# Kernel tuning notes

Hardware: AMD Instinct MI355X
Metric: run time of the kernel (lower is better)

## Reference

```python
import jax, jax.numpy as jnp
import numpy as np

N_NODES = 512
STATE_DIM = 32
MESSAGE_DIM = 32
H_MSG = 64
H_RO = 64
N_STEPS = 5


def setup_inputs() -> dict:
    key = jax.random.key(0)
    ks = jax.random.split(key, 20)
    s = 0.01  # torch init: normal(0, 0.01) weights, zero biases
    d, m = STATE_DIM, MESSAGE_DIM
    inp = {
        "J": jax.random.normal(ks[0], (N_NODES, N_NODES), jnp.float32),
        "b": jax.random.normal(ks[1], (N_NODES,), jnp.float32),
        # message-passing MLP
        "mp_W1": jax.random.normal(ks[2], (H_MSG, 2 * d + 3), jnp.float32) * s,
        "mp_b1": jnp.zeros((H_MSG,), jnp.float32),
        "mp_W2": jax.random.normal(ks[3], (H_MSG, H_MSG), jnp.float32) * s,
        "mp_b2": jnp.zeros((H_MSG,), jnp.float32),
        "mp_W3": jax.random.normal(ks[4], (m, H_MSG), jnp.float32) * s,
        "mp_b3": jnp.zeros((m,), jnp.float32),
        # GRU (input = state_dim + message_dim, hidden = state_dim); gate order r,z,n
        "gru_Wih": jax.random.normal(ks[5], (3 * d, d + m), jnp.float32) * 0.1,
        "gru_Whh": jax.random.normal(ks[6], (3 * d, d), jnp.float32) * 0.1,
        "gru_bih": jax.random.normal(ks[7], (3 * d,), jnp.float32) * 0.1,
        "gru_bhh": jax.random.normal(ks[8], (3 * d,), jnp.float32) * 0.1,
        # readout MLP
        "r_W1": jax.random.normal(ks[9], (H_RO, d), jnp.float32) * s,
        "r_b1": jnp.zeros((H_RO,), jnp.float32),
        "r_W2": jax.random.normal(ks[10], (H_RO, H_RO), jnp.float32) * s,
        "r_b2": jnp.zeros((H_RO,), jnp.float32),
        "r_W3": jax.random.normal(ks[11], (2, H_RO), jnp.float32) * s,
        "r_b3": jnp.zeros((2,), jnp.float32),
    }
    return inp


def reference(J, b, mp_W1, mp_b1, mp_W2, mp_b2, mp_W3, mp_b3,
              gru_Wih, gru_Whh, gru_bih, gru_bhh,
              r_W1, r_b1, r_W2, r_b2, r_W3, r_b3):
    n = J.shape[0]
    d = gru_Whh.shape[1]
    # split first message-layer weight by input segments to avoid building [n,n,2d+3]
    Wi, Wj = mp_W1[:, :d], mp_W1[:, d:2 * d]          # [H, d]
    wJ, wbi, wbj = mp_W1[:, 2 * d], mp_W1[:, 2 * d + 1], mp_W1[:, 2 * d + 2]  # [H]

    def step(h, _):
        # pre[i, j, :] = W1 @ cat(h_i, h_j, J_ij, b_i, b_j) + b1
        pre = ((h @ Wi.T)[:, None, :] + (h @ Wj.T)[None, :, :]
               + J[:, :, None] * wJ + b[:, None, None] * wbi
               + b[None, :, None] * wbj + mp_b1)          # [n, n, H]
        m1 = jax.nn.relu(pre)
        m2 = jax.nn.relu(m1 @ mp_W2.T + mp_b2)            # [n, n, H]
        msg = jax.nn.relu(m2 @ mp_W3.T + mp_b3)           # [n, n, M]
        msg_sum = msg.sum(axis=0)                         # sum over senders i -> [n, M]
        # GRU cell over all nodes (torch GRU, gate order r,z,n)
        x = jnp.concatenate([h, msg_sum], axis=-1)        # [n, d+M]
        gi = x @ gru_Wih.T + gru_bih                      # [n, 3d]
        gh = h @ gru_Whh.T + gru_bhh                      # [n, 3d]
        i_r, i_z, i_n = jnp.split(gi, 3, axis=-1)
        h_r, h_z, h_n = jnp.split(gh, 3, axis=-1)
        r = jax.nn.sigmoid(i_r + h_r)
        z = jax.nn.sigmoid(i_z + h_z)
        n_g = jnp.tanh(i_n + r * h_n)
        h_new = (1.0 - z) * n_g + z * h
        return h_new, None

    h0 = jnp.zeros((n, d), J.dtype)
    h, _ = jax.lax.scan(step, h0, None, length=N_STEPS)
    y = jax.nn.relu(h @ r_W1.T + r_b1)
    y = jax.nn.relu(y @ r_W2.T + r_b2)
    y = jax.nn.relu(y @ r_W3.T + r_b3)                    # [n, 2]
    return jax.nn.sigmoid(y)
```

## Files before the change

### kernel.cpp

```cpp
#include <hip/hip_runtime.h>
#include <math.h>

#define NN 512
#define SD 32
#define HM 64

typedef _Float16 f16x8 __attribute__((ext_vector_type(8)));
typedef float floatx4 __attribute__((ext_vector_type(4)));
typedef unsigned uintx4 __attribute__((ext_vector_type(4)));

#define OFF_HBS   0
#define OFF_M2L   73728
#define OFF_MSUM  92160
#define OFF_HPREV 93184
#define OFF_HS    93440
#define OFF_MSG   93696
#define OFF_GI    93952
#define OFF_GH    94720
#define LDS_TOTAL 95488

__device__ __forceinline__ float sigmoidf_(float x) {
    return 1.0f / (1.0f + __expf(-x));
}
__device__ __forceinline__ unsigned pkrtz(float a, float b) {
    unsigned r;
    asm("v_cvt_pkrtz_f16_f32 %0, %1, %2" : "=v"(r) : "v"(a), "v"(b));
    return r;
}
__device__ __forceinline__ unsigned pk_add(unsigned a, unsigned b) {
    unsigned r;
    asm("v_pk_add_f16 %0, %1, %2" : "=v"(r) : "v"(a), "v"(b));
    return r;
}
__device__ __forceinline__ unsigned pk_fma(unsigned a, unsigned b, unsigned c) {
    unsigned r;
    asm("v_pk_fma_f16 %0, %1, %2, %3" : "=v"(r) : "v"(a), "v"(b), "v"(c));
    return r;
}
__device__ __forceinline__ unsigned pk_relu(unsigned a) {
    unsigned r, z = 0u;
    asm("v_pk_max_f16 %0, %1, %2" : "=v"(r) : "v"(a), "v"(z));
    return r;
}

struct PParams {
    const float *J, *b, *mpW1, *mpb1, *mpW2, *mpW3, *Wih, *Whh, *rW1, *rW2;
    float *JT, *W1T, *WihT, *WhhT, *rW1T, *rW2T;
    unsigned *w2p, *w3p, *wjp, *hb0, *hjp0;
};

__global__ __launch_bounds__(256) void prep_kernel(PParams pp)
{
    __shared__ float tile[32][33];
    const int tid = threadIdx.x;
    const int b   = blockIdx.x;
    {
        int bx = b & 15, by = b >> 4;
        int tx = tid & 31, ty = tid >> 5;
        #pragma unroll
        for (int r = 0; r < 32; r += 8)
            tile[ty + r][tx] = pp.J[(by * 32 + ty + r) * NN + bx * 32 + tx];
        __syncthreads();
        #pragma unroll
        for (int r = 0; r < 32; r += 8)
            pp.JT[(bx * 32 + ty + r) * NN + by * 32 + tx] = tile[tx][ty + r];
    }
    if (b == 0 && tid < 64) {
        int l = tid, qq = l >> 4, cc = l & 15;
        for (int f = 0; f < 2; ++f)
            for (int t4 = 0; t4 < 4; ++t4) {
                const float* src = pp.mpW2 + (t4 * 16 + cc) * 64 + f * 32 + qq * 8;
                unsigned* dst = pp.w2p + ((f * 4 + t4) * 64 + l) * 4;
                for (int i = 0; i < 4; ++i) dst[i] = pkrtz(src[2 * i], src[2 * i + 1]);
            }
        for (int f = 0; f < 2; ++f)
            for (int t2 = 0; t2 < 2; ++t2) {
                const float* src = pp.mpW3 + (t2 * 16 + cc) * 64 + f * 32 + qq * 8;
                unsigned* dst = pp.w3p + ((f * 2 + t2) * 64 + l) * 4;
                for (int i = 0; i < 4; ++i) dst[i] = pkrtz(src[2 * i], src[2 * i + 1]);
            }
        for (int s = 0; s < 2; ++s) {
            unsigned* dst = pp.wjp + (s * 64 + l) * 4;
            for (int i = 0; i < 4; ++i) {
                int r0 = qq * 8 + 2 * i + s * 32;
                dst[i] = pkrtz(pp.mpW1[r0 * 67 + 64], pp.mpW1[(r0 + 1) * 67 + 64]);
            }
        }
    }
    if (b == 1)
        for (int n = tid; n < 64 * 67; n += 256) {
            int cc = n / 67, d = n % 67;
            pp.W1T[d * 64 + cc] = pp.mpW1[n];
        }
    if (b == 2)
        for (int n = tid; n < 96 * 64; n += 256)
            pp.WihT[(n & 63) * 96 + (n >> 6)] = pp.Wih[n];
    if (b == 3)
        for (int n = tid; n < 96 * 32; n += 256)
            pp.WhhT[(n & 31) * 96 + (n >> 5)] = pp.Whh[n];
    if (b == 4) {
        for (int n = tid; n < 64 * 32; n += 256)
            pp.rW1T[(n & 31) * 64 + (n >> 5)] = pp.rW1[n];
        for (int n = tid; n < 64 * 64; n += 256)
            pp.rW2T[(n & 63) * 64 + (n >> 6)] = pp.rW2[n];
    }
    if (b >= 16 && b < 144) {
        int jj = (b - 16) * 4 + (tid >> 6);
        int cc = tid & 63;
        float bj = pp.b[jj];
        float sj = bj * pp.mpW1[cc * 67 + 66] + pp.mpb1[cc];
        float si = bj * pp.mpW1[cc * 67 + 65];
        float sjp = __shfl(sj, cc ^ 1);
        float sip = __shfl(si, cc ^ 1);
        if (!(cc & 1)) {
            pp.hjp0[jj * 32 + (cc >> 1)] = pkrtz(sj, sjp);
            pp.hb0[jj * 32 + (cc >> 1)]  = pkrtz(si, sip);
        }
    }
}

struct SParams {
    const unsigned *hbR;  unsigned *hbW;
    const unsigned *hjR;  unsigned *hjW;
    const float *hR;      float *hW;
    const float *JT, *W1T, *WihT, *WhhT, *bih, *bhh, *mpb2, *mpb3, *b, *mpb1;
    const float *rW1T, *rW2T, *rW3, *rb1, *rb2, *rb3;
    const unsigned *w2p, *w3p, *wjp;
    float *out;
    int hzero, rdout;
};

__global__ __launch_bounds__(512, 1) void step_kernel(SParams s)
{
    extern __shared__ __align__(16) char smem[];
    char* hbS = smem + OFF_HBS;
    float (*msum)[32]   = (float(*)[32])(smem + OFF_MSUM);
    float (*hPrevS)[32] = (float(*)[32])(smem + OFF_HPREV);
    float (*hS)[32]     = (float(*)[32])(smem + OFF_HS);
    float (*msgS)[32]   = (float(*)[32])(smem + OFF_MSG);
    float (*giS)[96]    = (float(*)[96])(smem + OFF_GI);
    float (*ghS)[96]    = (float(*)[96])(smem + OFF_GH);

    const int tid  = threadIdx.x;
    const int lane = tid & 63;
    const int wave = tid >> 6;
    const int nsel = wave >> 2;
    const int nw   = wave & 3;
    const int j    = blockIdx.x * 2 + nsel;
    const int q    = lane >> 4;
    const int c    = lane & 15;
    char* m2Lw = smem + OFF_M2L + wave * 2304;

    {
        uintx4 cr[8];
        const uintx4* gp = (const uintx4*)s.hbR;
        #pragma unroll
        for (int k = 0; k < 8; ++k) cr[k] = gp[k * 512 + tid];
        #pragma unroll
        for (int k = 0; k < 8; ++k) {
            int row = k * 64 + (tid >> 3);
            *(uintx4*)(hbS + row * 144 + (tid & 7) * 16) = cr[k];
        }
    }
    if (tid < 64 && !s.hzero)
        hPrevS[tid >> 5][tid & 31] = s.hR[blockIdx.x * 64 + tid];
    __syncthreads();

    f16x8 Aw2[2][4], Aw3[2][2];
    #pragma unroll
    for (int f = 0; f < 2; ++f)
        #pragma unroll
        for (int t4 = 0; t4 < 4; ++t4)
            Aw2[f][t4] = __builtin_bit_cast(f16x8,
                ((const uintx4*)s.w2p)[(f * 4 + t4) * 64 + lane]);
    #pragma unroll
    for (int f = 0; f < 2; ++f)
        #pragma unroll
        for (int t2 = 0; t2 < 2; ++t2)
            Aw3[f][t2] = __builtin_bit_cast(f16x8,
                ((const uintx4*)s.w3p)[(f * 2 + t2) * 64 + lane]);
    uintx4 wja = ((const uintx4*)s.wjp)[lane];
    uintx4 wjb = ((const uintx4*)s.wjp)[64 + lane];
    uintx4 hja = ((const uintx4*)s.hjR)[j * 8 + q];
    uintx4 hjb = ((const uintx4*)s.hjR)[j * 8 + 4 + q];

    floatx4 b2i[4], b3i[2];
    #pragma unroll
    for (int t4 = 0; t4 < 4; ++t4)
        #pragma unroll
        for (int r = 0; r < 4; ++r) b2i[t4][r] = s.mpb2[t4 * 16 + q * 4 + r];
    #pragma unroll
    for (int t2 = 0; t2 < 2; ++t2)
        #pragma unroll
        for (int r = 0; r < 4; ++r) b3i[t2][r] = s.mpb3[t2 * 16 + q * 4 + r];

    const float jA = s.JT[j * NN + (8 * q + nw) * 16 + c];
    const float jB = s.JT[j * NN + (8 * q + 4 + nw) * 16 + c];

    float accf[2][4];
    #pragma unroll
    for (int t2 = 0; t2 < 2; ++t2)
        #pragma unroll
        for (int r = 0; r < 4; ++r) accf[t2][r] = 0.0f;

    auto edge_group = [&](int G, float Jv) {
        const char* rb = hbS + (G * 16 + c) * 144;
        uintx4 vlo = *(const uintx4*)(rb + q * 16);
        uintx4 vhi = *(const uintx4*)(rb + 64 + q * 16);
        const unsigned Jp = pkrtz(Jv, Jv);

        uintx4 a0u, a1u;
        #pragma unroll
        for (int i = 0; i < 4; ++i) {
            a0u[i] = pk_relu(pk_fma(Jp, wja[i], pk_add(vlo[i], hja[i])));
            a1u[i] = pk_relu(pk_fma(Jp, wjb[i], pk_add(vhi[i], hjb[i])));
        }
        f16x8 B0 = __builtin_bit_cast(f16x8, a0u);
        f16x8 B1 = __builtin_bit_cast(f16x8, a1u);

        floatx4 c1[4];
        #pragma unroll
        for (int t4 = 0; t4 < 4; ++t4) {
            c1[t4] = __builtin_amdgcn_mfma_f32_16x16x32_f16(Aw2[0][t4], B0, b2i[t4], 0, 0, 0);
            c1[t4] = __builtin_amdgcn_mfma_f32_16x16x32_f16(Aw2[1][t4], B1, c1[t4], 0, 0, 0);
        }
        #pragma unroll
        for (int t4 = 0; t4 < 4; ++t4) {
            unsigned p0 = pkrtz(fmaxf(c1[t4][0], 0.f), fmaxf(c1[t4][1], 0.f));
            unsigned p1 = pkrtz(fmaxf(c1[t4][2], 0.f), fmaxf(c1[t4][3], 0.f));
            *(uint2*)(m2Lw + c * 144 + t4 * 32 + q * 8) = make_uint2(p0, p1);
        }
        uintx4 rlo = *(const uintx4*)(m2Lw + c * 144 + q * 16);
        uintx4 rhi = *(const uintx4*)(m2Lw + c * 144 + 64 + q * 16);
        f16x8 B2lo = __builtin_bit_cast(f16x8, rlo);
        f16x8 B2hi = __builtin_bit_cast(f16x8, rhi);

        floatx4 c2[2];
        #pragma unroll
        for (int t2 = 0; t2 < 2; ++t2) {
            c2[t2] = __builtin_amdgcn_mfma_f32_16x16x32_f16(Aw3[0][t2], B2lo, b3i[t2], 0, 0, 0);
            c2[t2] = __builtin_amdgcn_mfma_f32_16x16x32_f16(Aw3[1][t2], B2hi, c2[t2], 0, 0, 0);
        }
        #pragma unroll
        for (int t2 = 0; t2 < 2; ++t2)
            #pragma unroll
            for (int r = 0; r < 4; ++r)
                accf[t2][r] += fmaxf(c2[t2][r], 0.0f);
    };

    #pragma unroll
    for (int k = 0; k < 4; ++k) {
        edge_group(8 * k + nw,     __shfl(jA, k * 16 + c));
        edge_group(8 * k + 4 + nw, __shfl(jB, k * 16 + c));
    }

    #pragma unroll
    for (int m = 1; m < 16; m <<= 1)
        #pragma unroll
        for (int t2 = 0; t2 < 2; ++t2)
            #pragma unroll
            for (int r = 0; r < 4; ++r)
                accf[t2][r] += __shfl_xor(accf[t2][r], m);
    if (c == 0) {
        #pragma unroll
        for (int t2 = 0; t2 < 2; ++t2)
            #pragma unroll
            for (int r = 0; r < 4; ++r)
                msum[wave][t2 * 16 + q * 4 + r] = accf[t2][r];
    }
    __syncthreads();

    if (tid < 64) {
        int node = tid >> 5, d = tid & 31;
        msgS[node][d] = msum[node * 4 + 0][d] + msum[node * 4 + 1][d] +
                        msum[node * 4 + 2][d] + msum[node * 4 + 3][d];
    }
    __syncthreads();

    if (tid < 192) {
        int node = tid / 96, r = tid % 96;
        float a  = s.bih[r];
        float bb = s.bhh[r];
        if (!s.hzero) {
            #pragma unroll
            for (int k = 0; k < 32; ++k) {
                float hv = hPrevS[node][k];
                a  = fmaf(hv, s.WihT[k * 96 + r], a);
                bb = fmaf(hv, s.WhhT[k * 96 + r], bb);
            }
        }
        #pragma unroll
        for (int k = 0; k < 32; ++k)
            a = fmaf(msgS[node][k], s.WihT[(32 + k) * 96 + r], a);
        giS[node][r] = a; ghS[node][r] = bb;
    }
    __syncthreads();

    if (tid < 64) {
        int node = tid >> 5, d = tid & 31;
        float r  = sigmoidf_(giS[node][d] + ghS[node][d]);
        float z  = sigmoidf_(giS[node][32 + d] + ghS[node][32 + d]);
        float ng = tanhf(giS[node][64 + d] + r * ghS[node][64 + d]);
        float hold = s.hzero ? 0.0f : hPrevS[node][d];
        float hv = (1.0f - z) * ng + z * hold;
        hS[node][d] = hv;
        s.hW[blockIdx.x * 64 + tid] = hv;
    }
    __syncthreads();

    if (!s.rdout) {
        if (tid < 128) {
            int node = tid >> 6, cc = tid & 63;
            int jj = blockIdx.x * 2 + node;
            float bj = s.b[jj];
            float si = bj * s.W1T[65 * 64 + cc];
            float sj = bj * s.W1T[66 * 64 + cc] + s.mpb1[cc];
            #pragma unroll
            for (int d = 0; d < 32; ++d) {
                float hv = hS[node][d];
                si = fmaf(hv, s.W1T[d * 64 + cc], si);
                sj = fmaf(hv, s.W1T[(32 + d) * 64 + cc], sj);
            }
            float sip = __shfl(si, lane ^ 1);
            float sjp = __shfl(sj, lane ^ 1);
            if (!(cc & 1)) {
                s.hbW[jj * 32 + (cc >> 1)] = pkrtz(si, sip);
                s.hjW[jj * 32 + (cc >> 1)] = pkrtz(sj, sjp);
            }
        }
    } else {
        if (wave < 2) {
            int node = wave;
            int jj = blockIdx.x * 2 + node;
            float y1 = s.rb1[lane];
            #pragma unroll
            for (int k = 0; k < 32; ++k)
                y1 = fmaf(hS[node][k], s.rW1T[k * 64 + lane], y1);
            y1 = fmaxf(y1, 0.0f);
            float y2 = s.rb2[lane];
            #pragma unroll
            for (int k = 0; k < 64; ++k)
                y2 = fmaf(__shfl(y1, k), s.rW2T[k * 64 + lane], y2);
            y2 = fmaxf(y2, 0.0f);
            float y3 = (lane < 2) ? s.rb3[lane] : 0.0f;
            #pragma unroll
            for (int k = 0; k < 64; ++k) {
                float v = __shfl(y2, k);
                if (lane < 2) y3 = fmaf(v, s.rW3[lane * 64 + k], y3);
            }
            if (lane < 2) s.out[jj * 2 + lane] = sigmoidf_(y3);
        }
    }
}

extern "C" void kernel_launch(void* const* d_in, const int* in_sizes, int n_in,
                              void* d_out, int out_size, void* d_ws, size_t ws_size,
                              hipStream_t stream)
{
    float* ws = (float*)d_ws;

    const float* J    = (const float*)d_in[0];
    const float* b    = (const float*)d_in[1];
    const float* mpW1 = (const float*)d_in[2];
    const float* mpb1 = (const float*)d_in[3];
    const float* mpW2 = (const float*)d_in[4];
    const float* mpb2 = (const float*)d_in[5];
    const float* mpW3 = (const float*)d_in[6];
    const float* mpb3 = (const float*)d_in[7];
    const float* Wih  = (const float*)d_in[8];
    const float* Whh  = (const float*)d_in[9];
    const float* bih  = (const float*)d_in[10];
    const float* bhh  = (const float*)d_in[11];
    const float* rW1  = (const float*)d_in[12];
    const float* rb1  = (const float*)d_in[13];
    const float* rW2  = (const float*)d_in[14];
    const float* rb2  = (const float*)d_in[15];
    const float* rW3  = (const float*)d_in[16];
    const float* rb3  = (const float*)d_in[17];

    float*    JT   = ws;
    float*    W1T  = ws + 262144;
    float*    WihT = ws + 266432;
    float*    WhhT = ws + 272576;
    float*    rW1T = ws + 275648;
    float*    rW2T = ws + 277696;
    unsigned* w2p  = (unsigned*)(ws + 281792);
    unsigned* w3p  = (unsigned*)(ws + 283840);
    unsigned* wjp  = (unsigned*)(ws + 284864);
    unsigned* hb0  = (unsigned*)(ws + 285376);
    unsigned* hb1  = (unsigned*)(ws + 301760);
    unsigned* hj0  = (unsigned*)(ws + 318144);
    unsigned* hj1  = (unsigned*)(ws + 334528);
    float*    h0   = ws + 350912;
    float*    h1   = ws + 367296;

    PParams pp;
    pp.J = J; pp.b = b; pp.mpW1 = mpW1; pp.mpb1 = mpb1; pp.mpW2 = mpW2;
    pp.mpW3 = mpW3; pp.Wih = Wih; pp.Whh = Whh; pp.rW1 = rW1; pp.rW2 = rW2;
    pp.JT = JT; pp.W1T = W1T; pp.WihT = WihT; pp.WhhT = WhhT;
    pp.rW1T = rW1T; pp.rW2T = rW2T;
    pp.w2p = w2p; pp.w3p = w3p; pp.wjp = wjp; pp.hb0 = hb0; pp.hjp0 = hj0;

    (void)hipFuncSetAttribute((const void*)step_kernel,
                              hipFuncAttributeMaxDynamicSharedMemorySize, LDS_TOTAL);

    prep_kernel<<<dim3(256), dim3(256), 0, stream>>>(pp);

    SParams s;
    s.JT = JT; s.W1T = W1T; s.WihT = WihT; s.WhhT = WhhT;
    s.bih = bih; s.bhh = bhh; s.mpb2 = mpb2; s.mpb3 = mpb3; s.b = b; s.mpb1 = mpb1;
    s.rW1T = rW1T; s.rW2T = rW2T; s.rW3 = rW3; s.rb1 = rb1; s.rb2 = rb2; s.rb3 = rb3;
    s.w2p = w2p; s.w3p = w3p; s.wjp = wjp;
    s.out = (float*)d_out;

    for (int t = 0; t < 5; ++t) {
        s.hbR = (t & 1) ? hb1 : hb0;
        s.hbW = (t & 1) ? hb0 : hb1;
        s.hjR = (t & 1) ? hj1 : hj0;
        s.hjW = (t & 1) ? hj0 : hj1;
        s.hR  = (t & 1) ? h0 : h1;
        s.hW  = (t & 1) ? h1 : h0;
        s.hzero = (t == 0);
        s.rdout = (t == 4);
        step_kernel<<<dim3(256), dim3(512), LDS_TOTAL, stream>>>(s);
    }
}
```

Measured before the change: 151.4 us.

## Fold prep kernel into first step kernel launch

Removes the separate prep kernel and does its preprocessing inside the first step_kernel launch (hzero). That launch reads the raw weights and J directly, converts them in-register or in LDS, and writes the transposed and packed buffers for later steps. This drops one kernel launch and its dependency gap. In exchange the first step does uncoalesced strided J reads and extra conversion work, and a few blocks carry the weight transposes.

New measurement: 153.1 us. Within noise of the previous version (+1.2%).

```diff
diff --git a/kernel.cpp b/kernel.cpp
--- a/kernel.cpp
+++ b/kernel.cpp
@@ -17,7 +17,9 @@
 #define OFF_MSG   93696
 #define OFF_GI    93952
 #define OFF_GH    94720
-#define LDS_TOTAL 95488
+#define OFF_HJPS  95488
+#define OFF_W65   96000
+#define LDS_TOTAL 96256
 
 __device__ __forceinline__ float sigmoidf_(float x) {
     return 1.0f / (1.0f + __expf(-x));
@@ -43,89 +45,15 @@
     return r;
 }
 
-struct PParams {
-    const float *J, *b, *mpW1, *mpb1, *mpW2, *mpW3, *Wih, *Whh, *rW1, *rW2;
-    float *JT, *W1T, *WihT, *WhhT, *rW1T, *rW2T;
-    unsigned *w2p, *w3p, *wjp, *hb0, *hjp0;
-};
-
-__global__ __launch_bounds__(256) void prep_kernel(PParams pp)
-{
-    __shared__ float tile[32][33];
-    const int tid = threadIdx.x;
-    const int b   = blockIdx.x;
-    {
-        int bx = b & 15, by = b >> 4;
-        int tx = tid & 31, ty = tid >> 5;
-        #pragma unroll
-        for (int r = 0; r < 32; r += 8)
-            tile[ty + r][tx] = pp.J[(by * 32 + ty + r) * NN + bx * 32 + tx];
-        __syncthreads();
-        #pragma unroll
-        for (int r = 0; r < 32; r += 8)
-            pp.JT[(bx * 32 + ty + r) * NN + by * 32 + tx] = tile[tx][ty + r];
-    }
-    if (b == 0 && tid < 64) {
-        int l = tid, qq = l >> 4, cc = l & 15;
-        for (int f = 0; f < 2; ++f)
-            for (int t4 = 0; t4 < 4; ++t4) {
-                const float* src = pp.mpW2 + (t4 * 16 + cc) * 64 + f * 32 + qq * 8;
-                unsigned* dst = pp.w2p + ((f * 4 + t4) * 64 + l) * 4;
-                for (int i = 0; i < 4; ++i) dst[i] = pkrtz(src[2 * i], src[2 * i + 1]);
-            }
-        for (int f = 0; f < 2; ++f)
-            for (int t2 = 0; t2 < 2; ++t2) {
-                const float* src = pp.mpW3 + (t2 * 16 + cc) * 64 + f * 32 + qq * 8;
-                unsigned* dst = pp.w3p + ((f * 2 + t2) * 64 + l) * 4;
-                for (int i = 0; i < 4; ++i) dst[i] = pkrtz(src[2 * i], src[2 * i + 1]);
-            }
-        for (int s = 0; s < 2; ++s) {
-            unsigned* dst = pp.wjp + (s * 64 + l) * 4;
-            for (int i = 0; i < 4; ++i) {
-                int r0 = qq * 8 + 2 * i + s * 32;
-                dst[i] = pkrtz(pp.mpW1[r0 * 67 + 64], pp.mpW1[(r0 + 1) * 67 + 64]);
-            }
-        }
-    }
-    if (b == 1)
-        for (int n = tid; n < 64 * 67; n += 256) {
-            int cc = n / 67, d = n % 67;
-            pp.W1T[d * 64 + cc] = pp.mpW1[n];
-        }
-    if (b == 2)
-        for (int n = tid; n < 96 * 64; n += 256)
-            pp.WihT[(n & 63) * 96 + (n >> 6)] = pp.Wih[n];
-    if (b == 3)
-        for (int n = tid; n < 96 * 32; n += 256)
-            pp.WhhT[(n & 31) * 96 + (n >> 5)] = pp.Whh[n];
-    if (b == 4) {
-        for (int n = tid; n < 64 * 32; n += 256)
-            pp.rW1T[(n & 31) * 64 + (n >> 5)] = pp.rW1[n];
-        for (int n = tid; n < 64 * 64; n += 256)
-            pp.rW2T[(n & 63) * 64 + (n >> 6)] = pp.rW2[n];
-    }
-    if (b >= 16 && b < 144) {
-        int jj = (b - 16) * 4 + (tid >> 6);
-        int cc = tid & 63;
-        float bj = pp.b[jj];
-        float sj = bj * pp.mpW1[cc * 67 + 66] + pp.mpb1[cc];
-        float si = bj * pp.mpW1[cc * 67 + 65];
-        float sjp = __shfl(sj, cc ^ 1);
-        float sip = __shfl(si, cc ^ 1);
-        if (!(cc & 1)) {
-            pp.hjp0[jj * 32 + (cc >> 1)] = pkrtz(sj, sjp);
-            pp.hb0[jj * 32 + (cc >> 1)]  = pkrtz(si, sip);
-        }
-    }
-}
-
 struct SParams {
     const unsigned *hbR;  unsigned *hbW;
     const unsigned *hjR;  unsigned *hjW;
     const float *hR;      float *hW;
-    const float *JT, *W1T, *WihT, *WhhT, *bih, *bhh, *mpb2, *mpb3, *b, *mpb1;
-    const float *rW1T, *rW2T, *rW3, *rb1, *rb2, *rb3;
-    const unsigned *w2p, *w3p, *wjp;
+    float *JT, *W1T, *WihT, *WhhT, *rW1T, *rW2T;
+    unsigned *w2p, *w3p, *wjp;
+    const float *J, *mpW1, *mpb1, *mpW2, *mpb2, *mpW3, *mpb3;
+    const float *Wih, *Whh, *bih, *bhh, *b;
+    const float *rW1, *rW2, *rW3, *rb1, *rb2, *rb3;
     float *out;
     int hzero, rdout;
 };
@@ -140,6 +68,8 @@
     float (*msgS)[32]   = (float(*)[32])(smem + OFF_MSG);
     float (*giS)[96]    = (float(*)[96])(smem + OFF_GI);
     float (*ghS)[96]    = (float(*)[96])(smem + OFF_GH);
+    float (*hjpS)[64]   = (float(*)[64])(smem + OFF_HJPS);
+    float* w65S         = (float*)(smem + OFF_W65);
 
     const int tid  = threadIdx.x;
     const int lane = tid & 63;
@@ -151,7 +81,68 @@
     const int c    = lane & 15;
     char* m2Lw = smem + OFF_M2L + wave * 2304;
 
-    {
+    if (s.hzero) {
+        if (blockIdx.x == 1) {
+            for (int n = tid; n < 64 * 67; n += 512) {
+                int cc = n / 67, d = n % 67;
+                s.W1T[d * 64 + cc] = s.mpW1[n];
+            }
+        } else if (blockIdx.x == 2) {
+            for (int n = tid; n < 96 * 64; n += 512)
+                s.WihT[(n & 63) * 96 + (n >> 6)] = s.Wih[n];
+        } else if (blockIdx.x == 3) {
+            for (int n = tid; n < 96 * 32; n += 512)
+                s.WhhT[(n & 31) * 96 + (n >> 5)] = s.Whh[n];
+        } else if (blockIdx.x == 4) {
+            for (int n = tid; n < 64 * 32; n += 512)
+                s.rW1T[(n & 31) * 64 + (n >> 5)] = s.rW1[n];
+            for (int n = tid; n < 64 * 64; n += 512)
+                s.rW2T[(n & 63) * 64 + (n >> 6)] = s.rW2[n];
+        } else if (blockIdx.x == 5 && tid < 64) {
+            int l = tid, qq = l >> 4, cc = l & 15;
+            for (int f = 0; f < 2; ++f)
+                for (int t4 = 0; t4 < 4; ++t4) {
+                    const float* src = s.mpW2 + (t4 * 16 + cc) * 64 + f * 32 + qq * 8;
+                    unsigned* dst = s.w2p + ((f * 4 + t4) * 64 + l) * 4;
+                    for (int i = 0; i < 4; ++i) dst[i] = pkrtz(src[2 * i], src[2 * i + 1]);
+                }
+            for (int f = 0; f < 2; ++f)
+                for (int t2 = 0; t2 < 2; ++t2) {
+                    const float* src = s.mpW3 + (t2 * 16 + cc) * 64 + f * 32 + qq * 8;
+                    unsigned* dst = s.w3p + ((f * 2 + t2) * 64 + l) * 4;
+                    for (int i = 0; i < 4; ++i) dst[i] = pkrtz(src[2 * i], src[2 * i + 1]);
+                }
+            for (int s2 = 0; s2 < 2; ++s2) {
+                unsigned* dst = s.wjp + (s2 * 64 + l) * 4;
+                for (int i = 0; i < 4; ++i) {
+                    int r0 = qq * 8 + 2 * i + s2 * 32;
+                    dst[i] = pkrtz(s.mpW1[r0 * 67 + 64], s.mpW1[(r0 + 1) * 67 + 64]);
+                }
+            }
+        }
+        if (tid < 64) w65S[tid] = s.mpW1[tid * 67 + 65];
+        if (tid < 128) {
+            int node = tid >> 6, cc = tid & 63;
+            int jj = blockIdx.x * 2 + node;
+            float bj = s.b[jj];
+            hjpS[node][cc] = bj * s.mpW1[cc * 67 + 66] + s.mpb1[cc];
+        }
+        __syncthreads();
+        {
+            float bi = s.b[tid];
+            unsigned* dst = (unsigned*)(hbS + tid * 144);
+            #pragma unroll
+            for (int k8 = 0; k8 < 8; ++k8) {
+                uintx4 v;
+                #pragma unroll
+                for (int i = 0; i < 4; ++i) {
+                    int k = k8 * 4 + i;
+                    v[i] = pkrtz(bi * w65S[2 * k], bi * w65S[2 * k + 1]);
+                }
+                *(uintx4*)(dst + k8 * 4) = v;
+            }
+        }
+    } else {
         uintx4 cr[8];
         const uintx4* gp = (const uintx4*)s.hbR;
         #pragma unroll
@@ -161,28 +152,57 @@
             int row = k * 64 + (tid >> 3);
             *(uintx4*)(hbS + row * 144 + (tid & 7) * 16) = cr[k];
         }
-    }
-    if (tid < 64 && !s.hzero)
-        hPrevS[tid >> 5][tid & 31] = s.hR[blockIdx.x * 64 + tid];
+        if (tid < 64)
+            hPrevS[tid >> 5][tid & 31] = s.hR[blockIdx.x * 64 + tid];
+    }
     __syncthreads();
 
     f16x8 Aw2[2][4], Aw3[2][2];
-    #pragma unroll
-    for (int f = 0; f < 2; ++f)
-        #pragma unroll
-        for (int t4 = 0; t4 < 4; ++t4)
-            Aw2[f][t4] = __builtin_bit_cast(f16x8,
-                ((const uintx4*)s.w2p)[(f * 4 + t4) * 64 + lane]);
-    #pragma unroll
-    for (int f = 0; f < 2; ++f)
-        #pragma unroll
-        for (int t2 = 0; t2 < 2; ++t2)
-            Aw3[f][t2] = __builtin_bit_cast(f16x8,
-                ((const uintx4*)s.w3p)[(f * 2 + t2) * 64 + lane]);
-    uintx4 wja = ((const uintx4*)s.wjp)[lane];
-    uintx4 wjb = ((const uintx4*)s.wjp)[64 + lane];
-    uintx4 hja = ((const uintx4*)s.hjR)[j * 8 + q];
-    uintx4 hjb = ((const uintx4*)s.hjR)[j * 8 + 4 + q];
+    uintx4 wja, wjb, hja, hjb;
+    if (s.hzero) {
+        #pragma unroll
+        for (int f = 0; f < 2; ++f)
+            #pragma unroll
+            for (int t4 = 0; t4 < 4; ++t4) {
+                const float* src = s.mpW2 + (t4 * 16 + c) * 64 + f * 32 + q * 8;
+                #pragma unroll
+                for (int i = 0; i < 8; ++i) Aw2[f][t4][i] = (_Float16)src[i];
+            }
+        #pragma unroll
+        for (int f = 0; f < 2; ++f)
+            #pragma unroll
+            for (int t2 = 0; t2 < 2; ++t2) {
+                const float* src = s.mpW3 + (t2 * 16 + c) * 64 + f * 32 + q * 8;
+                #pragma unroll
+                for (int i = 0; i < 8; ++i) Aw3[f][t2][i] = (_Float16)src[i];
+            }
+        #pragma unroll
+        for (int i = 0; i < 4; ++i) {
+            wja[i] = pkrtz(s.mpW1[(q * 8 + 2 * i) * 67 + 64],
+                           s.mpW1[(q * 8 + 2 * i + 1) * 67 + 64]);
+            wjb[i] = pkrtz(s.mpW1[(q * 8 + 2 * i + 32) * 67 + 64],
+                           s.mpW1[(q * 8 + 2 * i + 33) * 67 + 64]);
+            hja[i] = pkrtz(hjpS[nsel][q * 8 + 2 * i], hjpS[nsel][q * 8 + 2 * i + 1]);
+            hjb[i] = pkrtz(hjpS[nsel][q * 8 + 2 * i + 32], hjpS[nsel][q * 8 + 2 * i + 33]);
+        }
+    } else {
+        #pragma unroll
+        for (int f = 0; f < 2; ++f)
+            #pragma unroll
+            for (int t4 = 0; t4 < 4; ++t4)
+                Aw2[f][t4] = __builtin_bit_cast(f16x8,
+                    ((const uintx4*)s.w2p)[(f * 4 + t4) * 64 + lane]);
+        #pragma unroll
+        for (int f = 0; f < 2; ++f)
+            #pragma unroll
+            for (int t2 = 0; t2 < 2; ++t2)
+                Aw3[f][t2] = __builtin_bit_cast(f16x8,
+                    ((const uintx4*)s.w3p)[(f * 2 + t2) * 64 + lane]);
+        wja = ((const uintx4*)s.wjp)[lane];
+        wjb = ((const uintx4*)s.wjp)[64 + lane];
+        hja = ((const uintx4*)s.hjR)[j * 8 + q];
+        hjb = ((const uintx4*)s.hjR)[j * 8 + 4 + q];
+    }
 
     floatx4 b2i[4], b3i[2];
     #pragma unroll
@@ -194,8 +214,16 @@
         #pragma unroll
         for (int r = 0; r < 4; ++r) b3i[t2][r] = s.mpb3[t2 * 16 + q * 4 + r];
 
-    const float jA = s.JT[j * NN + (8 * q + nw) * 16 + c];
-    const float jB = s.JT[j * NN + (8 * q + 4 + nw) * 16 + c];
+    float jA, jB;
+    if (s.hzero) {
+        jA = s.J[((8 * q + nw) * 16 + c) * NN + j];
+        jB = s.J[((8 * q + 4 + nw) * 16 + c) * NN + j];
+        s.JT[j * NN + (8 * q + nw) * 16 + c] = jA;
+        s.JT[j * NN + (8 * q + 4 + nw) * 16 + c] = jB;
+    } else {
+        jA = s.JT[j * NN + (8 * q + nw) * 16 + c];
+        jB = s.JT[j * NN + (8 * q + 4 + nw) * 16 + c];
+    }
 
     float accf[2][4];
     #pragma unroll
@@ -288,10 +316,14 @@
                 a  = fmaf(hv, s.WihT[k * 96 + r], a);
                 bb = fmaf(hv, s.WhhT[k * 96 + r], bb);
             }
-        }
-        #pragma unroll
-        for (int k = 0; k < 32; ++k)
-            a = fmaf(msgS[node][k], s.WihT[(32 + k) * 96 + r], a);
+            #pragma unroll
+            for (int k = 0; k < 32; ++k)
+                a = fmaf(msgS[node][k], s.WihT[(32 + k) * 96 + r], a);
+        } else {
+            #pragma unroll
+            for (int k = 0; k < 32; ++k)
+                a = fmaf(msgS[node][k], s.Wih[r * 64 + 32 + k], a);
+        }
         giS[node][r] = a; ghS[node][r] = bb;
     }
     __syncthreads();
@@ -313,13 +345,25 @@
             int node = tid >> 6, cc = tid & 63;
             int jj = blockIdx.x * 2 + node;
             float bj = s.b[jj];
-            float si = bj * s.W1T[65 * 64 + cc];
-            float sj = bj * s.W1T[66 * 64 + cc] + s.mpb1[cc];
-            #pragma unroll
-            for (int d = 0; d < 32; ++d) {
-                float hv = hS[node][d];
-                si = fmaf(hv, s.W1T[d * 64 + cc], si);
-                sj = fmaf(hv, s.W1T[(32 + d) * 64 + cc], sj);
+            float si, sj;
+            if (s.hzero) {
+                si = bj * s.mpW1[cc * 67 + 65];
+                sj = bj * s.mpW1[cc * 67 + 66] + s.mpb1[cc];
+                #pragma unroll
+                for (int d = 0; d < 32; ++d) {
+                    float hv = hS[node][d];
+                    si = fmaf(hv, s.mpW1[cc * 67 + d], si);
+                    sj = fmaf(hv, s.mpW1[cc * 67 + 32 + d], sj);
+                }
+            } else {
+                si = bj * s.W1T[65 * 64 + cc];
+                sj = bj * s.W1T[66 * 64 + cc] + s.mpb1[cc];
+                #pragma unroll
+                for (int d = 0; d < 32; ++d) {
+                    float hv = hS[node][d];
+                    si = fmaf(hv, s.W1T[d * 64 + cc], si);
+                    sj = fmaf(hv, s.W1T[(32 + d) * 64 + cc], sj);
+                }
             }
             float sip = __shfl(si, lane ^ 1);
             float sjp = __shfl(sj, lane ^ 1);
@@ -359,59 +403,45 @@
 {
     float* ws = (float*)d_ws;
 
-    const float* J    = (const float*)d_in[0];
-    const float* b    = (const float*)d_in[1];
-    const float* mpW1 = (const float*)d_in[2];
-    const float* mpb1 = (const float*)d_in[3];
-    const float* mpW2 = (const float*)d_in[4];
-    const float* mpb2 = (const float*)d_in[5];
-    const float* mpW3 = (const float*)d_in[6];
-    const float* mpb3 = (const float*)d_in[7];
-    const float* Wih  = (const float*)d_in[8];
-    const float* Whh  = (const float*)d_in[9];
-    const float* bih  = (const float*)d_in[10];
-    const float* bhh  = (const float*)d_in[11];
-    const float* rW1  = (const float*)d_in[12];
-    const float* rb1  = (const float*)d_in[13];
-    const float* rW2  = (const float*)d_in[14];
-    const float* rb2  = (const float*)d_in[15];
-    const float* rW3  = (const float*)d_in[16];
-    const float* rb3  = (const float*)d_in[17];
-
-    float*    JT   = ws;
-    float*    W1T  = ws + 262144;
-    float*    WihT = ws + 266432;
-    float*    WhhT = ws + 272576;
-    float*    rW1T = ws + 275648;
-    float*    rW2T = ws + 277696;
-    unsigned* w2p  = (unsigned*)(ws + 281792);
-    unsigned* w3p  = (unsigned*)(ws + 283840);
-    unsigned* wjp  = (unsigned*)(ws + 284864);
-    unsigned* hb0  = (unsigned*)(ws + 285376);
-    unsigned* hb1  = (unsigned*)(ws + 301760);
-    unsigned* hj0  = (unsigned*)(ws + 318144);
-    unsigned* hj1  = (unsigned*)(ws + 334528);
-    float*    h0   = ws + 350912;
-    float*    h1   = ws + 367296;
-
-    PParams pp;
-    pp.J = J; pp.b = b; pp.mpW1 = mpW1; pp.mpb1 = mpb1; pp.mpW2 = mpW2;
-    pp.mpW3 = mpW3; pp.Wih = Wih; pp.Whh = Whh; pp.rW1 = rW1; pp.rW2 = rW2;
-    pp.JT = JT; pp.W1T = W1T; pp.WihT = WihT; pp.WhhT = WhhT;
-    pp.rW1T = rW1T; pp.rW2T = rW2T;
-    pp.w2p = w2p; pp.w3p = w3p; pp.wjp = wjp; pp.hb0 = hb0; pp.hjp0 = hj0;
+    SParams s;
+    s.J    = (const float*)d_in[0];
+    s.b    = (const float*)d_in[1];
+    s.mpW1 = (const float*)d_in[2];
+    s.mpb1 = (const float*)d_in[3];
+    s.mpW2 = (const float*)d_in[4];
+    s.mpb2 = (const float*)d_in[5];
+    s.mpW3 = (const float*)d_in[6];
+    s.mpb3 = (const float*)d_in[7];
+    s.Wih  = (const float*)d_in[8];
+    s.Whh  = (const float*)d_in[9];
+    s.bih  = (const float*)d_in[10];
+    s.bhh  = (const float*)d_in[11];
+    s.rW1  = (const float*)d_in[12];
+    s.rb1  = (const float*)d_in[13];
+    s.rW2  = (const float*)d_in[14];
+    s.rb2  = (const float*)d_in[15];
+    s.rW3  = (const float*)d_in[16];
+    s.rb3  = (const float*)d_in[17];
+    s.out  = (float*)d_out;
+
+    s.JT   = ws;
+    s.W1T  = ws + 262144;
+    s.WihT = ws + 266432;
+    s.WhhT = ws + 272576;
+    s.rW1T = ws + 275648;
+    s.rW2T = ws + 277696;
+    s.w2p  = (unsigned*)(ws + 281792);
+    s.w3p  = (unsigned*)(ws + 283840);
+    s.wjp  = (unsigned*)(ws + 284864);
+    unsigned* hb0 = (unsigned*)(ws + 285376);
+    unsigned* hb1 = (unsigned*)(ws + 301760);
+    unsigned* hj0 = (unsigned*)(ws + 318144);
+    unsigned* hj1 = (unsigned*)(ws + 334528);
+    float*    h0  = ws + 350912;
+    float*    h1  = ws + 367296;
 
     (void)hipFuncSetAttribute((const void*)step_kernel,
                               hipFuncAttributeMaxDynamicSharedMemorySize, LDS_TOTAL);
-
-    prep_kernel<<<dim3(256), dim3(256), 0, stream>>>(pp);
-
-    SParams s;
-    s.JT = JT; s.W1T = W1T; s.WihT = WihT; s.WhhT = WhhT;
-    s.bih = bih; s.bhh = bhh; s.mpb2 = mpb2; s.mpb3 = mpb3; s.b = b; s.mpb1 = mpb1;
-    s.rW1T = rW1T; s.rW2T = rW2T; s.rW3 = rW3; s.rb1 = rb1; s.rb2 = rb2; s.rb3 = rb3;
-    s.w2p = w2p; s.w3p = w3p; s.wjp = wjp;
-    s.out = (float*)d_out;
 
     for (int t = 0; t < 5; ++t) {
         s.hbR = (t & 1) ? hb1 : hb0;
```
